# Optimization experiments

Measured on AMD Instinct MI355X. Metric: run time of the kernel, lower is better.

## Reference

```python
import jax, jax.numpy as jnp
import numpy as np

NUM_CAPSULE = 16
DIM_CAPSULE = 32
ROUTINGS = 3


def setup_inputs() -> dict:
    key = jax.random.key(0)
    k1, k2 = jax.random.split(key)
    B, S, D = 256, 512, 256  # batch, input_num_capsule, input_dim_capsule
    x = jax.random.normal(k1, (B, S, D), dtype=jnp.float32)
    # xavier-normal-ish init for W [input_dim_capsule, num_capsule*dim_capsule]
    O = NUM_CAPSULE * DIM_CAPSULE
    std = float(np.sqrt(2.0 / (D + O)))
    W = jax.random.normal(k2, (D, O), dtype=jnp.float32) * std
    return {"x": x, "W": W}


def _squash(v, axis=-1):
    # NOTE: faithful to source: divides by sqrt(||v||^2 + 1e-7) (unit-norm style)
    s = jnp.sum(v * v, axis=axis, keepdims=True)
    return v / jnp.sqrt(s + 1e-7)


def reference(x, W):
    B, S, D = x.shape
    # u_hat: [B, num_capsule, S, dim_capsule]
    u_hat = jnp.einsum('bsd,do->bso', x, W)
    u_hat = u_hat.reshape(B, S, NUM_CAPSULE, DIM_CAPSULE).transpose(0, 2, 1, 3)
    b = jnp.zeros((B, NUM_CAPSULE, S), dtype=u_hat.dtype)
    outputs = None
    for i in range(ROUTINGS):
        # softmax over the num_capsule axis (source permutes then softmax dim=2)
        c = jax.nn.softmax(b, axis=1)  # [B, nc, S]
        outputs = _squash(jnp.einsum('bns,bnsd->bnd', c, u_hat))  # [B, nc, dc]
        if i < ROUTINGS - 1:
            b = jnp.einsum('bnd,bnsd->bns', outputs, u_hat)
    return outputs.reshape(-1, NUM_CAPSULE * DIM_CAPSULE)
```

## Files before the change

kernel.cpp:

```cpp
#include <hip/hip_runtime.h>


#define S_ 512
#define D_ 256
#define O_ 512

typedef __attribute__((ext_vector_type(8))) short short8;
typedef __attribute__((ext_vector_type(4))) float floatx4;

__device__ __forceinline__ unsigned short f2b(float f) {
  union { float ff; unsigned int i; } v; v.ff = f;
  unsigned int u = v.i;
  return (unsigned short)((u + 0x7FFFu + ((u >> 16) & 1u)) >> 16);
}

__global__ __launch_bounds__(512, 2) void caps_kernel(
    const float* __restrict__ x, const float* __restrict__ W,
    float* __restrict__ out)
{
  __shared__ __align__(16) float bl[16 * 520];
  __shared__ __align__(16) float ytmp[16 * 260];
  __shared__ __align__(16) unsigned short zb[16 * 264];
  __shared__ __align__(16) float outp[O_];

  const int tid  = threadIdx.x;
  const int wave = tid >> 6;
  const int lane = tid & 63;
  const float* xb = x + (size_t)blockIdx.x * (S_ * D_);

  for (int it = 0; it < 3; ++it) {
    if (it == 0) {
      float a0 = 0.f, a1 = 0.f, a2 = 0.f, a3 = 0.f;
      #pragma unroll 4
      for (int r = 0; r < 64; ++r) {
        const int s = (wave << 6) + r;
        const float4 xv = *(const float4*)(xb + s * D_ + (lane << 2));
        a0 += xv.x; a1 += xv.y; a2 += xv.z; a3 += xv.w;
      }
      *(float4*)(bl + wave * 520 + (lane << 2)) = make_float4(a0, a1, a2, a3);
      __syncthreads();
      if (tid < 256) {
        float v = 0.f;
        #pragma unroll
        for (int w = 0; w < 8; ++w) v += bl[w * 520 + tid];
        v *= 0.0625f;
        #pragma unroll
        for (int n = 0; n < 16; ++n) ytmp[n * 260 + tid] = v;
      }
      __syncthreads();
    } else {
      {
        const int s = tid;
        float vv[16];
        float m = -1e30f;
        #pragma unroll
        for (int n = 0; n < 16; ++n) { vv[n] = bl[n * 520 + s]; m = fmaxf(m, vv[n]); }
        float sum = 0.f;
        #pragma unroll
        for (int n = 0; n < 16; ++n) { vv[n] = __expf(vv[n] - m); sum += vv[n]; }
        const float inv = 1.f / sum;
        #pragma unroll
        for (int n = 0; n < 16; ++n) bl[n * 520 + s] = vv[n] * inv;
      }
      __syncthreads();
      float acc[16][4];
      #pragma unroll
      for (int n = 0; n < 16; ++n) { acc[n][0]=0.f; acc[n][1]=0.f; acc[n][2]=0.f; acc[n][3]=0.f; }
      for (int g = 0; g < 16; ++g) {
        const int s0 = (wave << 6) + (g << 2);
        float cc[16][4];
        #pragma unroll
        for (int n = 0; n < 16; ++n) {
          const float4 c4 = *(const float4*)(bl + n * 520 + s0);
          cc[n][0] = c4.x; cc[n][1] = c4.y; cc[n][2] = c4.z; cc[n][3] = c4.w;
        }
        #pragma unroll
        for (int j = 0; j < 4; ++j) {
          const float4 xv = *(const float4*)(xb + (s0 + j) * D_ + (lane << 2));
          #pragma unroll
          for (int n = 0; n < 16; ++n) {
            acc[n][0] += cc[n][j] * xv.x; acc[n][1] += cc[n][j] * xv.y;
            acc[n][2] += cc[n][j] * xv.z; acc[n][3] += cc[n][j] * xv.w;
          }
        }
      }
      for (int rr = 0; rr < 8; ++rr) {
        if (wave == rr) {
          #pragma unroll
          for (int n = 0; n < 16; ++n) {
            float4* p = (float4*)(ytmp + n * 260 + (lane << 2));
            if (rr == 0) { *p = make_float4(acc[n][0], acc[n][1], acc[n][2], acc[n][3]); }
            else { float4 v = *p; v.x += acc[n][0]; v.y += acc[n][1]; v.z += acc[n][2]; v.w += acc[n][3]; *p = v; }
          }
        }
        __syncthreads();
      }
    }

    {
      const int o = tid;
      const int n = o >> 5;
      float a = 0.f;
      for (int Db = 0; Db < 32; ++Db) {
        const float4 y0 = *(const float4*)(ytmp + n * 260 + (Db << 3));
        const float4 y1 = *(const float4*)(ytmp + n * 260 + (Db << 3) + 4);
        const float* wp = W + (size_t)(Db << 3) * O_ + o;
        a += y0.x * wp[0 * O_]; a += y0.y * wp[1 * O_];
        a += y0.z * wp[2 * O_]; a += y0.w * wp[3 * O_];
        a += y1.x * wp[4 * O_]; a += y1.y * wp[5 * O_];
        a += y1.z * wp[6 * O_]; a += y1.w * wp[7 * O_];
      }
      float ss = a * a;
      #pragma unroll
      for (int off = 1; off < 32; off <<= 1) ss += __shfl_xor(ss, off, 64);
      const float v = a / sqrtf(ss + 1e-7f);
      outp[o] = v;
      if (it == 2) out[(size_t)blockIdx.x * O_ + o] = v;
    }
    __syncthreads();

    if (it < 2) {
      {
        const int obase = lane << 3;
        const int n_ln  = lane >> 2;
        float ov[8];
        #pragma unroll
        for (int j = 0; j < 8; ++j) ov[j] = outp[obase + j];
        for (int r = 0; r < 32; ++r) {
          const int Dd = (wave << 5) + r;
          const float4 w0 = *(const float4*)(W + (size_t)Dd * O_ + obase);
          const float4 w1 = *(const float4*)(W + (size_t)Dd * O_ + obase + 4);
          float a = w0.x * ov[0] + w0.y * ov[1] + w0.z * ov[2] + w0.w * ov[3]
                  + w1.x * ov[4] + w1.y * ov[5] + w1.z * ov[6] + w1.w * ov[7];
          a += __shfl_xor(a, 1, 64);
          a += __shfl_xor(a, 2, 64);
          if ((lane & 3) == 0) zb[n_ln * 264 + Dd] = f2b(a);
        }
      }
      __syncthreads();
      const int l15 = lane & 15, l4 = lane >> 4;
      for (int t = 0; t < 4; ++t) {
        const int s0 = ((wave << 2) + t) << 4;
        floatx4 C = {0.f, 0.f, 0.f, 0.f};
        #pragma unroll
        for (int k = 0; k < 8; ++k) {
          const short8 A = *(const short8*)(zb + l15 * 264 + (k << 5) + (l4 << 3));
          const float* xp = xb + (s0 + l15) * D_ + (k << 5) + (l4 << 3);
          const float4 xv0 = *(const float4*)xp;
          const float4 xv1 = *(const float4*)(xp + 4);
          short8 Bf;
          Bf[0] = (short)f2b(xv0.x); Bf[1] = (short)f2b(xv0.y);
          Bf[2] = (short)f2b(xv0.z); Bf[3] = (short)f2b(xv0.w);
          Bf[4] = (short)f2b(xv1.x); Bf[5] = (short)f2b(xv1.y);
          Bf[6] = (short)f2b(xv1.z); Bf[7] = (short)f2b(xv1.w);
          C = __builtin_amdgcn_mfma_f32_16x16x32_bf16(A, Bf, C, 0, 0, 0);
        }
        #pragma unroll
        for (int rg = 0; rg < 4; ++rg)
          bl[((l4 << 2) + rg) * 520 + s0 + l15] = C[rg];
      }
      __syncthreads();
    }
  }
}

extern "C" void kernel_launch(void* const* d_in, const int* in_sizes, int n_in,
                              void* d_out, int out_size, void* d_ws, size_t ws_size,
                              hipStream_t stream) {
  const float* x = (const float*)d_in[0];
  const float* W = (const float*)d_in[1];
  float* out = (float*)d_out;
  (void)in_sizes; (void)n_in; (void)out_size; (void)d_ws; (void)ws_size;
  caps_kernel<<<256, 512, 0, stream>>>(x, W, out);
}
```

Baseline: 300.4 us.

## Fuse logits MFMA, softmax and weighted sum per wave tile, atomically reduce into shared

Moves the bf16 MFMA computation of routing logits from the end of each iteration into the start of the next one. The softmax over capsules is now done in registers with cross-lane shuffles, and the coefficients go to a small per-wave shared tile that feeds the weighted x accumulation directly. The 16x520 logits buffer, the block-wide softmax pass and its barrier all go away. The 8-step serialized cross-wave reduction with a barrier per step is replaced by shared-memory atomicAdds into a zeroed ytmp. The trade is extra atomic traffic and the x tile being read twice within the same phase.

```diff
diff --git a/kernel.cpp b/kernel.cpp
--- a/kernel.cpp
+++ b/kernel.cpp
@@ -18,7 +18,7 @@
     const float* __restrict__ x, const float* __restrict__ W,
     float* __restrict__ out)
 {
-  __shared__ __align__(16) float bl[16 * 520];
+  __shared__ __align__(16) float bl[8 * 256];
   __shared__ __align__(16) float ytmp[16 * 260];
   __shared__ __align__(16) unsigned short zb[16 * 264];
   __shared__ __align__(16) float outp[O_];
@@ -26,7 +26,9 @@
   const int tid  = threadIdx.x;
   const int wave = tid >> 6;
   const int lane = tid & 63;
+  const int l15  = lane & 15, l4 = lane >> 4;
   const float* xb = x + (size_t)blockIdx.x * (S_ * D_);
+  float* ct = bl + wave * 256;
 
   for (int it = 0; it < 3; ++it) {
     if (it == 0) {
@@ -37,64 +39,79 @@
         const float4 xv = *(const float4*)(xb + s * D_ + (lane << 2));
         a0 += xv.x; a1 += xv.y; a2 += xv.z; a3 += xv.w;
       }
-      *(float4*)(bl + wave * 520 + (lane << 2)) = make_float4(a0, a1, a2, a3);
+      *(float4*)(bl + wave * 256 + (lane << 2)) = make_float4(a0, a1, a2, a3);
       __syncthreads();
       if (tid < 256) {
         float v = 0.f;
         #pragma unroll
-        for (int w = 0; w < 8; ++w) v += bl[w * 520 + tid];
+        for (int w = 0; w < 8; ++w) v += bl[w * 256 + tid];
         v *= 0.0625f;
         #pragma unroll
         for (int n = 0; n < 16; ++n) ytmp[n * 260 + tid] = v;
       }
       __syncthreads();
     } else {
-      {
-        const int s = tid;
-        float vv[16];
-        float m = -1e30f;
+      for (int i = tid; i < 16 * 260; i += 512) ytmp[i] = 0.f;
+      __syncthreads();
+
+      float yacc[16][4];
+      #pragma unroll
+      for (int n = 0; n < 16; ++n) { yacc[n][0]=0.f; yacc[n][1]=0.f; yacc[n][2]=0.f; yacc[n][3]=0.f; }
+
+      for (int t = 0; t < 4; ++t) {
+        const int s0 = (wave << 6) + (t << 4);
+        floatx4 C = {0.f, 0.f, 0.f, 0.f};
         #pragma unroll
-        for (int n = 0; n < 16; ++n) { vv[n] = bl[n * 520 + s]; m = fmaxf(m, vv[n]); }
-        float sum = 0.f;
-        #pragma unroll
-        for (int n = 0; n < 16; ++n) { vv[n] = __expf(vv[n] - m); sum += vv[n]; }
-        const float inv = 1.f / sum;
-        #pragma unroll
-        for (int n = 0; n < 16; ++n) bl[n * 520 + s] = vv[n] * inv;
-      }
-      __syncthreads();
-      float acc[16][4];
-      #pragma unroll
-      for (int n = 0; n < 16; ++n) { acc[n][0]=0.f; acc[n][1]=0.f; acc[n][2]=0.f; acc[n][3]=0.f; }
-      for (int g = 0; g < 16; ++g) {
-        const int s0 = (wave << 6) + (g << 2);
-        float cc[16][4];
-        #pragma unroll
-        for (int n = 0; n < 16; ++n) {
-          const float4 c4 = *(const float4*)(bl + n * 520 + s0);
-          cc[n][0] = c4.x; cc[n][1] = c4.y; cc[n][2] = c4.z; cc[n][3] = c4.w;
+        for (int k = 0; k < 8; ++k) {
+          const short8 A = *(const short8*)(zb + l15 * 264 + (k << 5) + (l4 << 3));
+          const float* xp = xb + (s0 + l15) * D_ + (k << 5) + (l4 << 3);
+          const float4 xv0 = *(const float4*)xp;
+          const float4 xv1 = *(const float4*)(xp + 4);
+          short8 Bf;
+          Bf[0] = (short)f2b(xv0.x); Bf[1] = (short)f2b(xv0.y);
+          Bf[2] = (short)f2b(xv0.z); Bf[3] = (short)f2b(xv0.w);
+          Bf[4] = (short)f2b(xv1.x); Bf[5] = (short)f2b(xv1.y);
+          Bf[6] = (short)f2b(xv1.z); Bf[7] = (short)f2b(xv1.w);
+          C = __builtin_amdgcn_mfma_f32_16x16x32_bf16(A, Bf, C, 0, 0, 0);
         }
-        #pragma unroll
-        for (int j = 0; j < 4; ++j) {
-          const float4 xv = *(const float4*)(xb + (s0 + j) * D_ + (lane << 2));
+        float m = fmaxf(fmaxf(C[0], C[1]), fmaxf(C[2], C[3]));
+        m = fmaxf(m, __shfl_xor(m, 16, 64));
+        m = fmaxf(m, __shfl_xor(m, 32, 64));
+        float e0 = __expf(C[0] - m), e1 = __expf(C[1] - m);
+        float e2 = __expf(C[2] - m), e3 = __expf(C[3] - m);
+        float sm = e0 + e1 + e2 + e3;
+        sm += __shfl_xor(sm, 16, 64);
+        sm += __shfl_xor(sm, 32, 64);
+        const float inv = 1.f / sm;
+        *(float4*)(ct + l15 * 16 + (l4 << 2)) = make_float4(e0*inv, e1*inv, e2*inv, e3*inv);
+        __asm__ volatile("s_waitcnt lgkmcnt(0)" ::: "memory");
+        #pragma unroll 4
+        for (int s = 0; s < 16; ++s) {
+          const float4 xv = *(const float4*)(xb + (s0 + s) * D_ + (lane << 2));
+          const float4 c0 = *(const float4*)(ct + s * 16);
+          const float4 c1 = *(const float4*)(ct + s * 16 + 4);
+          const float4 c2 = *(const float4*)(ct + s * 16 + 8);
+          const float4 c3 = *(const float4*)(ct + s * 16 + 12);
+          float cf[16];
+          cf[0]=c0.x;  cf[1]=c0.y;  cf[2]=c0.z;  cf[3]=c0.w;
+          cf[4]=c1.x;  cf[5]=c1.y;  cf[6]=c1.z;  cf[7]=c1.w;
+          cf[8]=c2.x;  cf[9]=c2.y;  cf[10]=c2.z; cf[11]=c2.w;
+          cf[12]=c3.x; cf[13]=c3.y; cf[14]=c3.z; cf[15]=c3.w;
           #pragma unroll
           for (int n = 0; n < 16; ++n) {
-            acc[n][0] += cc[n][j] * xv.x; acc[n][1] += cc[n][j] * xv.y;
-            acc[n][2] += cc[n][j] * xv.z; acc[n][3] += cc[n][j] * xv.w;
+            yacc[n][0] += cf[n] * xv.x; yacc[n][1] += cf[n] * xv.y;
+            yacc[n][2] += cf[n] * xv.z; yacc[n][3] += cf[n] * xv.w;
           }
         }
       }
-      for (int rr = 0; rr < 8; ++rr) {
-        if (wave == rr) {
-          #pragma unroll
-          for (int n = 0; n < 16; ++n) {
-            float4* p = (float4*)(ytmp + n * 260 + (lane << 2));
-            if (rr == 0) { *p = make_float4(acc[n][0], acc[n][1], acc[n][2], acc[n][3]); }
-            else { float4 v = *p; v.x += acc[n][0]; v.y += acc[n][1]; v.z += acc[n][2]; v.w += acc[n][3]; *p = v; }
-          }
-        }
-        __syncthreads();
+      #pragma unroll
+      for (int jj = 0; jj < 4; ++jj) {
+        const int j = ((lane >> 3) + jj) & 3;
+        #pragma unroll
+        for (int n = 0; n < 16; ++n)
+          atomicAdd(&ytmp[n * 260 + (lane << 2) + j], yacc[n][j]);
       }
+      __syncthreads();
     }
 
     {
@@ -120,44 +137,20 @@
     __syncthreads();
 
     if (it < 2) {
-      {
-        const int obase = lane << 3;
-        const int n_ln  = lane >> 2;
-        float ov[8];
-        #pragma unroll
-        for (int j = 0; j < 8; ++j) ov[j] = outp[obase + j];
-        for (int r = 0; r < 32; ++r) {
-          const int Dd = (wave << 5) + r;
-          const float4 w0 = *(const float4*)(W + (size_t)Dd * O_ + obase);
-          const float4 w1 = *(const float4*)(W + (size_t)Dd * O_ + obase + 4);
-          float a = w0.x * ov[0] + w0.y * ov[1] + w0.z * ov[2] + w0.w * ov[3]
-                  + w1.x * ov[4] + w1.y * ov[5] + w1.z * ov[6] + w1.w * ov[7];
-          a += __shfl_xor(a, 1, 64);
-          a += __shfl_xor(a, 2, 64);
-          if ((lane & 3) == 0) zb[n_ln * 264 + Dd] = f2b(a);
-        }
-      }
-      __syncthreads();
-      const int l15 = lane & 15, l4 = lane >> 4;
-      for (int t = 0; t < 4; ++t) {
-        const int s0 = ((wave << 2) + t) << 4;
-        floatx4 C = {0.f, 0.f, 0.f, 0.f};
-        #pragma unroll
-        for (int k = 0; k < 8; ++k) {
-          const short8 A = *(const short8*)(zb + l15 * 264 + (k << 5) + (l4 << 3));
-          const float* xp = xb + (s0 + l15) * D_ + (k << 5) + (l4 << 3);
-          const float4 xv0 = *(const float4*)xp;
-          const float4 xv1 = *(const float4*)(xp + 4);
-          short8 Bf;
-          Bf[0] = (short)f2b(xv0.x); Bf[1] = (short)f2b(xv0.y);
-          Bf[2] = (short)f2b(xv0.z); Bf[3] = (short)f2b(xv0.w);
-          Bf[4] = (short)f2b(xv1.x); Bf[5] = (short)f2b(xv1.y);
-          Bf[6] = (short)f2b(xv1.z); Bf[7] = (short)f2b(xv1.w);
-          C = __builtin_amdgcn_mfma_f32_16x16x32_bf16(A, Bf, C, 0, 0, 0);
-        }
-        #pragma unroll
-        for (int rg = 0; rg < 4; ++rg)
-          bl[((l4 << 2) + rg) * 520 + s0 + l15] = C[rg];
+      const int obase = lane << 3;
+      const int n_ln  = lane >> 2;
+      float ov[8];
+      #pragma unroll
+      for (int jq = 0; jq < 8; ++jq) ov[jq] = outp[obase + jq];
+      for (int r = 0; r < 32; ++r) {
+        const int Dd = (wave << 5) + r;
+        const float4 w0 = *(const float4*)(W + (size_t)Dd * O_ + obase);
+        const float4 w1 = *(const float4*)(W + (size_t)Dd * O_ + obase + 4);
+        float a = w0.x * ov[0] + w0.y * ov[1] + w0.z * ov[2] + w0.w * ov[3]
+                + w1.x * ov[4] + w1.y * ov[5] + w1.z * ov[6] + w1.w * ov[7];
+        a += __shfl_xor(a, 1, 64);
+        a += __shfl_xor(a, 2, 64);
+        if ((lane & 3) == 0) zb[n_ln * 264 + Dd] = f2b(a);
       }
       __syncthreads();
     }
```

Measured after the change: 380.9 us. +26.8%, slower.
